# Performance work log

Hardware: AMD Instinct MI355X
Metric: run time of the kernel (lower is better)

## Reference

```python
import jax, jax.numpy as jnp
import numpy as np

B, L, C = 16, 4096, 9          # batch, max chars, max candidate spans per char (2+3+4)
DI, DO, V = 512, 128, 96       # char hidden, attention/pos-embed dim, pos-BEM vocab


def setup_inputs() -> dict:
    key = jax.random.key(0)
    k0, k1, k2, k3, k4, k5 = jax.random.split(key, 6)
    input_context = jax.random.normal(k0, (B, L, DI), jnp.float32)
    W = jax.random.normal(k1, (DO, DI), jnp.float32) / np.sqrt(DI).astype(np.float32)
    pos_embed = jax.random.normal(k2, (V, DO), jnp.float32)
    cand_idx = jax.random.randint(k3, (B, L, C), 0, V, dtype=jnp.int32)
    cand_mask = jax.random.randint(k4, (B, L, C), 0, 2, dtype=jnp.int32).astype(bool)
    word_seq_len = jax.random.randint(k5, (B,), L // 2, L + 1, dtype=jnp.int32)
    return {
        'input_context': input_context,
        'W': W,
        'pos_embed': pos_embed,
        'cand_idx': cand_idx,
        'cand_mask': cand_mask,
        'word_seq_len': word_seq_len,
    }


def reference(input_context, W, pos_embed, cand_idx, cand_mask, word_seq_len):
    # 'general' attention: score_c = cand_c . (W x_char)
    q = jnp.einsum('bld,od->blo', input_context, W)          # [B, L, DO]
    cand = pos_embed[cand_idx]                               # [B, L, C, DO] gather
    scores = jnp.einsum('blco,blo->blc', cand, q)            # [B, L, C]
    neg = jnp.finfo(scores.dtype).min
    attn = jax.nn.softmax(jnp.where(cand_mask, scores, neg), axis=-1)
    ctx = jnp.einsum('blc,blco->blo', attn, cand)            # [B, L, DO]
    # chars with no matched candidate -> zeros(output_size); pad beyond seq_len -> zeros
    has_cand = cand_mask.any(axis=-1, keepdims=True)         # [B, L, 1]
    in_len = jnp.arange(L, dtype=word_seq_len.dtype)[None, :, None] < word_seq_len[:, None, None]
    return jnp.where(has_cand & in_len, ctx, jnp.zeros((), ctx.dtype))
```

## Files before the change

kernel.cpp:

```cpp
#include <hip/hip_runtime.h>
#include <hip/hip_bf16.h>
#include <hip/hip_fp16.h>
#include <cfloat>

#define BB   16
#define LL   4096
#define CC   9
#define DIN  512
#define DOUT 128
#define VV   96

#define PWLD 520
#define PELD 136

typedef _Float16 h2 __attribute__((ext_vector_type(2)));

#if defined(__has_builtin)
#if __has_builtin(__builtin_amdgcn_fdot2)
#define FDOT2(a, b, c) __builtin_amdgcn_fdot2((a), (b), (c), false)
#endif
#endif
#ifndef FDOT2
__device__ __forceinline__ float FDOT2(h2 a, h2 b, float c) {
    return c + (float)a[0] * (float)b[0] + (float)a[1] * (float)b[1];
}
#endif

__device__ __forceinline__ h2 pack_h2(float lo, float hi) {
    return __builtin_bit_cast(h2, __builtin_amdgcn_cvt_pkrtz(lo, hi));
}

__global__ __launch_bounds__(128)
void pw_kernel(const float* __restrict__ W,
               const float* __restrict__ PE,
               __half*      __restrict__ PW)
{
    const int v = blockIdx.x;
    const int k = blockIdx.y * 128 + threadIdx.x;
    const float* per = PE + v * DOUT;
    float a = 0.f;
    #pragma unroll 8
    for (int o = 0; o < DOUT; ++o)
        a = fmaf(per[o], W[(size_t)o * DIN + k], a);
    PW[(size_t)v * DIN + k] = __float2half_rn(a);
}

__global__ __launch_bounds__(256)
void peh_kernel(const float* __restrict__ PE, __half* __restrict__ PEh)
{
    const int i = blockIdx.x * 256 + threadIdx.x;
    float2 f = ((const float2*)PE)[i];
    ((__half2*)PEh)[i] = __floats2half2_rn(f.x, f.y);
}

__global__ __launch_bounds__(1024, 1)
void attn_kernel(const float*  __restrict__ X,
                 const __half* __restrict__ PW,
                 const __half* __restrict__ PEh,
                 const int*    __restrict__ CIDX,
                 const int*    __restrict__ CMASK,
                 const int*    __restrict__ SLEN,
                 float*        __restrict__ OUT)
{
    __shared__ __half lds_pw[VV * PWLD];
    __shared__ __half lds_pe[VV * PELD];

    const int t = threadIdx.x;

    #pragma unroll
    for (int it = 0; it < 6; ++it) {
        int chunk = t + it * 1024;
        int v = chunk >> 6, kq = chunk & 63;
        uint4 d = *(const uint4*)(PW + (size_t)v * DIN + kq * 8);
        *(uint4*)&lds_pw[v * PWLD + kq * 8] = d;
    }
    {
        int v = t >> 4, kq = t & 15;
        if (t < 1536)
            *(uint4*)&lds_pe[v * PELD + kq * 8] =
                *(const uint4*)(PEh + (size_t)v * DOUT + kq * 8);
        int c2 = t + 1024;
        if (c2 < 1536) {
            int v2 = c2 >> 4, k2 = c2 & 15;
            *(uint4*)&lds_pe[v2 * PELD + k2 * 8] =
                *(const uint4*)(PEh + (size_t)v2 * DOUT + k2 * 8);
        }
    }
    __syncthreads();

    const int lane = t & 63;
    const int il   = lane & 15;
    const int slot = t >> 4;
    const int rowbase = blockIdx.x * 128;

    #pragma unroll
    for (int iter = 0; iter < 2; ++iter) {
        const int row = rowbase + iter * 64 + slot;
        const int  b     = row >> 12;
        const int  l     = row & (LL - 1);
        const bool inlen = l < SLEN[b];

        int ci[CC], vmw[CC];
        #pragma unroll
        for (int c = 0; c < CC; ++c) ci[c]  = CIDX[(size_t)row * CC + c];
        #pragma unroll
        for (int c = 0; c < CC; ++c) vmw[c] = CMASK[(size_t)row * CC + c];

        const float* xr = X + (size_t)row * DIN;
        float4 xf[8];
        #pragma unroll
        for (int j = 0; j < 4; ++j) {
            xf[j * 2 + 0] = *(const float4*)(xr + il * 8 + 128 * j);
            xf[j * 2 + 1] = *(const float4*)(xr + il * 8 + 128 * j + 4);
        }
        h2 xh[16];
        #pragma unroll
        for (int q = 0; q < 8; ++q) {
            xh[q * 2 + 0] = pack_h2(xf[q].x, xf[q].y);
            xh[q * 2 + 1] = pack_h2(xf[q].z, xf[q].w);
        }

        float sc[CC];
        #pragma unroll
        for (int c = 0; c < CC; ++c) sc[c] = 0.f;
        #pragma unroll
        for (int j = 0; j < 4; ++j) {
            #pragma unroll
            for (int c = 0; c < CC; ++c) {
                uint4 pwb = *(const uint4*)&lds_pw[ci[c] * PWLD + j * 128 + il * 8];
                h2 p0 = __builtin_bit_cast(h2, pwb.x);
                h2 p1 = __builtin_bit_cast(h2, pwb.y);
                h2 p2 = __builtin_bit_cast(h2, pwb.z);
                h2 p3 = __builtin_bit_cast(h2, pwb.w);
                float s = sc[c];
                s = FDOT2(xh[j * 4 + 0], p0, s);
                s = FDOT2(xh[j * 4 + 1], p1, s);
                s = FDOT2(xh[j * 4 + 2], p2, s);
                s = FDOT2(xh[j * 4 + 3], p3, s);
                sc[c] = s;
            }
        }
        #pragma unroll
        for (int c = 0; c < CC; ++c) {
            float s = sc[c];
            s += __shfl_xor(s, 1);
            s += __shfl_xor(s, 2);
            s += __shfl_xor(s, 4);
            s += __shfl_xor(s, 8);
            sc[c] = s;
        }

        bool any = false;
        float mx = -FLT_MAX;
        #pragma unroll
        for (int c = 0; c < CC; ++c)
            if (vmw[c]) { mx = fmaxf(mx, sc[c]); any = true; }
        float e[CC];
        float den = 0.f;
        #pragma unroll
        for (int c = 0; c < CC; ++c) {
            e[c] = vmw[c] ? __expf(sc[c] - mx) : 0.f;
            den += e[c];
        }
        const float scale = (any && inlen) ? (1.f / den) : 0.f;

        float o[8];
        #pragma unroll
        for (int j = 0; j < 8; ++j) o[j] = 0.f;
        #pragma unroll
        for (int c = 0; c < CC; ++c) {
            const float w = e[c];
            uint4 peb = *(const uint4*)&lds_pe[ci[c] * PELD + il * 8];
            h2 q0 = __builtin_bit_cast(h2, peb.x);
            h2 q1 = __builtin_bit_cast(h2, peb.y);
            h2 q2 = __builtin_bit_cast(h2, peb.z);
            h2 q3 = __builtin_bit_cast(h2, peb.w);
            o[0] = fmaf(w, (float)q0[0], o[0]); o[1] = fmaf(w, (float)q0[1], o[1]);
            o[2] = fmaf(w, (float)q1[0], o[2]); o[3] = fmaf(w, (float)q1[1], o[3]);
            o[4] = fmaf(w, (float)q2[0], o[4]); o[5] = fmaf(w, (float)q2[1], o[5]);
            o[6] = fmaf(w, (float)q3[0], o[6]); o[7] = fmaf(w, (float)q3[1], o[7]);
        }

        float* op = OUT + (size_t)row * DOUT + il * 8;
        *(float4*)op       = make_float4(o[0] * scale, o[1] * scale, o[2] * scale, o[3] * scale);
        *(float4*)(op + 4) = make_float4(o[4] * scale, o[5] * scale, o[6] * scale, o[7] * scale);
    }
}

extern "C" void kernel_launch(void* const* d_in, const int* in_sizes, int n_in,
                              void* d_out, int out_size, void* d_ws, size_t ws_size,
                              hipStream_t stream) {
    const float* X  = (const float*)d_in[0];
    const float* W  = (const float*)d_in[1];
    const float* PE = (const float*)d_in[2];
    const int*   CI = (const int*)d_in[3];
    const int*   CM = (const int*)d_in[4];
    const int*   SL = (const int*)d_in[5];
    float* OUT = (float*)d_out;
    __half* PW  = (__half*)d_ws;
    __half* PEh = (__half*)d_ws + (size_t)VV * DIN;

    hipLaunchKernelGGL(pw_kernel, dim3(VV, 4), dim3(128), 0, stream, W, PE, PW);
    hipLaunchKernelGGL(peh_kernel, dim3((VV * DOUT / 2) / 256), dim3(256), 0, stream, PE, PEh);

    const int rows = BB * LL;
    hipLaunchKernelGGL(attn_kernel, dim3(rows / 128), dim3(1024), 0, stream,
                       X, PW, PEh, CI, CM, SL, OUT);
}
```

Before: 45.24 us.

## Fold PE fp16 conversion into pw_kernel and double-buffer row loads

Merges the PE-to-half conversion into the PW precompute kernel, which removes one kernel launch. The attention kernel now processes 256 rows per block (4 iterations) instead of 128, so each block amortizes its LDS table fill over more rows. It also prefetches the next row's indices, mask and X slice into registers while computing the current row. Launch bounds now request 4 blocks per SM, but each block uses about 126 KB of LDS, so occupancy is probably still limited to one block. The double-buffered registers raise VGPR pressure.

```diff
diff --git a/kernel.cpp b/kernel.cpp
--- a/kernel.cpp
+++ b/kernel.cpp
@@ -33,7 +33,8 @@
 __global__ __launch_bounds__(128)
 void pw_kernel(const float* __restrict__ W,
                const float* __restrict__ PE,
-               __half*      __restrict__ PW)
+               __half*      __restrict__ PW,
+               __half*      __restrict__ PEh)
 {
     const int v = blockIdx.x;
     const int k = blockIdx.y * 128 + threadIdx.x;
@@ -43,17 +44,11 @@
     for (int o = 0; o < DOUT; ++o)
         a = fmaf(per[o], W[(size_t)o * DIN + k], a);
     PW[(size_t)v * DIN + k] = __float2half_rn(a);
-}
-
-__global__ __launch_bounds__(256)
-void peh_kernel(const float* __restrict__ PE, __half* __restrict__ PEh)
-{
-    const int i = blockIdx.x * 256 + threadIdx.x;
-    float2 f = ((const float2*)PE)[i];
-    ((__half2*)PEh)[i] = __floats2half2_rn(f.x, f.y);
-}
-
-__global__ __launch_bounds__(1024, 1)
+    if (blockIdx.y == 0)
+        PEh[(size_t)v * DOUT + threadIdx.x] = __float2half_rn(per[threadIdx.x]);
+}
+
+__global__ __launch_bounds__(1024, 4)
 void attn_kernel(const float*  __restrict__ X,
                  const __half* __restrict__ PW,
                  const __half* __restrict__ PEh,
@@ -75,10 +70,11 @@
         *(uint4*)&lds_pw[v * PWLD + kq * 8] = d;
     }
     {
-        int v = t >> 4, kq = t & 15;
-        if (t < 1536)
+        if (t < 1536) {
+            int v = t >> 4, kq = t & 15;
             *(uint4*)&lds_pe[v * PELD + kq * 8] =
                 *(const uint4*)(PEh + (size_t)v * DOUT + kq * 8);
+        }
         int c2 = t + 1024;
         if (c2 < 1536) {
             int v2 = c2 >> 4, k2 = c2 & 15;
@@ -91,43 +87,65 @@
     const int lane = t & 63;
     const int il   = lane & 15;
     const int slot = t >> 4;
-    const int rowbase = blockIdx.x * 128;
+    const int rowbase = blockIdx.x * 256;
+
+    int    ci[2][CC];
+    int    vmw[2][CC];
+    float4 xf[2][8];
+
+    {
+        const int row = rowbase + slot;
+        #pragma unroll
+        for (int c = 0; c < CC; ++c) ci[0][c]  = CIDX[(size_t)row * CC + c];
+        #pragma unroll
+        for (int c = 0; c < CC; ++c) vmw[0][c] = CMASK[(size_t)row * CC + c];
+        const float* xr = X + (size_t)row * DIN;
+        #pragma unroll
+        for (int j = 0; j < 4; ++j) {
+            xf[0][j * 2 + 0] = *(const float4*)(xr + il * 8 + 128 * j);
+            xf[0][j * 2 + 1] = *(const float4*)(xr + il * 8 + 128 * j + 4);
+        }
+    }
 
     #pragma unroll
-    for (int iter = 0; iter < 2; ++iter) {
-        const int row = rowbase + iter * 64 + slot;
+    for (int i = 0; i < 4; ++i) {
+        const int cur = i & 1;
+        const int nxt = cur ^ 1;
+
+        if (i < 3) {
+            const int rown = rowbase + (i + 1) * 64 + slot;
+            #pragma unroll
+            for (int c = 0; c < CC; ++c) ci[nxt][c]  = CIDX[(size_t)rown * CC + c];
+            #pragma unroll
+            for (int c = 0; c < CC; ++c) vmw[nxt][c] = CMASK[(size_t)rown * CC + c];
+            const float* xrn = X + (size_t)rown * DIN;
+            #pragma unroll
+            for (int j = 0; j < 4; ++j) {
+                xf[nxt][j * 2 + 0] = *(const float4*)(xrn + il * 8 + 128 * j);
+                xf[nxt][j * 2 + 1] = *(const float4*)(xrn + il * 8 + 128 * j + 4);
+            }
+        }
+
+        const int row = rowbase + i * 64 + slot;
         const int  b     = row >> 12;
         const int  l     = row & (LL - 1);
         const bool inlen = l < SLEN[b];
 
-        int ci[CC], vmw[CC];
-        #pragma unroll
-        for (int c = 0; c < CC; ++c) ci[c]  = CIDX[(size_t)row * CC + c];
-        #pragma unroll
-        for (int c = 0; c < CC; ++c) vmw[c] = CMASK[(size_t)row * CC + c];
-
-        const float* xr = X + (size_t)row * DIN;
-        float4 xf[8];
+        h2 xh[16];
+        #pragma unroll
+        for (int q = 0; q < 8; ++q) {
+            xh[q * 2 + 0] = pack_h2(xf[cur][q].x, xf[cur][q].y);
+            xh[q * 2 + 1] = pack_h2(xf[cur][q].z, xf[cur][q].w);
+        }
+
+        float sc[CC];
+        #pragma unroll
+        for (int c = 0; c < CC; ++c) sc[c] = 0.f;
         #pragma unroll
         for (int j = 0; j < 4; ++j) {
-            xf[j * 2 + 0] = *(const float4*)(xr + il * 8 + 128 * j);
-            xf[j * 2 + 1] = *(const float4*)(xr + il * 8 + 128 * j + 4);
-        }
-        h2 xh[16];
-        #pragma unroll
-        for (int q = 0; q < 8; ++q) {
-            xh[q * 2 + 0] = pack_h2(xf[q].x, xf[q].y);
-            xh[q * 2 + 1] = pack_h2(xf[q].z, xf[q].w);
-        }
-
-        float sc[CC];
-        #pragma unroll
-        for (int c = 0; c < CC; ++c) sc[c] = 0.f;
-        #pragma unroll
-        for (int j = 0; j < 4; ++j) {
             #pragma unroll
             for (int c = 0; c < CC; ++c) {
-                uint4 pwb = *(const uint4*)&lds_pw[ci[c] * PWLD + j * 128 + il * 8];
+                uint4 pwb = *(const uint4*)&lds_pw[ci[cur][c] * PWLD + j * 128 + il * 8];
                 h2 p0 = __builtin_bit_cast(h2, pwb.x);
                 h2 p1 = __builtin_bit_cast(h2, pwb.y);
                 h2 p2 = __builtin_bit_cast(h2, pwb.z);
@@ -154,12 +172,12 @@
         float mx = -FLT_MAX;
         #pragma unroll
         for (int c = 0; c < CC; ++c)
-            if (vmw[c]) { mx = fmaxf(mx, sc[c]); any = true; }
+            if (vmw[cur][c]) { mx = fmaxf(mx, sc[c]); any = true; }
         float e[CC];
         float den = 0.f;
         #pragma unroll
         for (int c = 0; c < CC; ++c) {
-            e[c] = vmw[c] ? __expf(sc[c] - mx) : 0.f;
+            e[c] = vmw[cur][c] ? __expf(sc[c] - mx) : 0.f;
             den += e[c];
         }
         const float scale = (any && inlen) ? (1.f / den) : 0.f;
@@ -170,7 +188,7 @@
         #pragma unroll
         for (int c = 0; c < CC; ++c) {
             const float w = e[c];
-            uint4 peb = *(const uint4*)&lds_pe[ci[c] * PELD + il * 8];
+            uint4 peb = *(const uint4*)&lds_pe[ci[cur][c] * PELD + il * 8];
             h2 q0 = __builtin_bit_cast(h2, peb.x);
             h2 q1 = __builtin_bit_cast(h2, peb.y);
             h2 q2 = __builtin_bit_cast(h2, peb.z);
@@ -200,10 +218,9 @@
     __half* PW  = (__half*)d_ws;
     __half* PEh = (__half*)d_ws + (size_t)VV * DIN;
 
-    hipLaunchKernelGGL(pw_kernel, dim3(VV, 4), dim3(128), 0, stream, W, PE, PW);
-    hipLaunchKernelGGL(peh_kernel, dim3((VV * DOUT / 2) / 256), dim3(256), 0, stream, PE, PEh);
+    hipLaunchKernelGGL(pw_kernel, dim3(VV, 4), dim3(128), 0, stream, W, PE, PW, PEh);
 
     const int rows = BB * LL;
-    hipLaunchKernelGGL(attn_kernel, dim3(rows / 128), dim3(1024), 0, stream,
+    hipLaunchKernelGGL(attn_kernel, dim3(rows / 256), dim3(1024), 0, stream,
                        X, PW, PEh, CI, CM, SL, OUT);
 }
```

Measured after the change: 45.81 us. Within noise of the previous version (+1.3%).

## Compute all-vocab scores with MFMA instead of per-candidate fdot2 gathers

Applied to the files above, without the earlier changes.

Replaces the per-candidate gathered fdot2 scoring with a dense MFMA 16x16x32 f16 GEMM of each row against all 96 precomputed PE·W vectors. The scores go to LDS (reusing the PW buffer) and each row's 9 candidates are picked from there. The x loads are software-pipelined with four register buffers, the PE fp16 conversion is folded into pw_kernel, and each block now handles 256 rows. This trades about 10x redundant FLOPs, which the matrix cores absorb, for far fewer scattered LDS reads, at the cost of extra syncs and an LDS round trip for the scores.

```diff
diff --git a/kernel.cpp b/kernel.cpp
--- a/kernel.cpp
+++ b/kernel.cpp
@@ -10,30 +10,23 @@
 #define DOUT 128
 #define VV   96
 
-#define PWLD 520
+#define BLD  536
+#define SLD  97
 #define PELD 136
-
-typedef _Float16 h2 __attribute__((ext_vector_type(2)));
-
-#if defined(__has_builtin)
-#if __has_builtin(__builtin_amdgcn_fdot2)
-#define FDOT2(a, b, c) __builtin_amdgcn_fdot2((a), (b), (c), false)
-#endif
-#endif
-#ifndef FDOT2
-__device__ __forceinline__ float FDOT2(h2 a, h2 b, float c) {
-    return c + (float)a[0] * (float)b[0] + (float)a[1] * (float)b[1];
-}
-#endif
-
-__device__ __forceinline__ h2 pack_h2(float lo, float hi) {
-    return __builtin_bit_cast(h2, __builtin_amdgcn_cvt_pkrtz(lo, hi));
+#define BBYTES (VV * BLD * 2)
+
+typedef _Float16 f16x8 __attribute__((ext_vector_type(8)));
+typedef __attribute__((ext_vector_type(4))) float f32x4;
+
+__device__ __forceinline__ unsigned int pk2(float lo, float hi) {
+    return __builtin_bit_cast(unsigned int, __builtin_amdgcn_cvt_pkrtz(lo, hi));
 }
 
 __global__ __launch_bounds__(128)
 void pw_kernel(const float* __restrict__ W,
                const float* __restrict__ PE,
-               __half*      __restrict__ PW)
+               __half*      __restrict__ PW,
+               __half*      __restrict__ PEh)
 {
     const int v = blockIdx.x;
     const int k = blockIdx.y * 128 + threadIdx.x;
@@ -43,17 +36,11 @@
     for (int o = 0; o < DOUT; ++o)
         a = fmaf(per[o], W[(size_t)o * DIN + k], a);
     PW[(size_t)v * DIN + k] = __float2half_rn(a);
-}
-
-__global__ __launch_bounds__(256)
-void peh_kernel(const float* __restrict__ PE, __half* __restrict__ PEh)
-{
-    const int i = blockIdx.x * 256 + threadIdx.x;
-    float2 f = ((const float2*)PE)[i];
-    ((__half2*)PEh)[i] = __floats2half2_rn(f.x, f.y);
-}
-
-__global__ __launch_bounds__(1024, 1)
+    if (blockIdx.y == 0)
+        PEh[(size_t)v * DOUT + threadIdx.x] = __float2half_rn(per[threadIdx.x]);
+}
+
+__global__ __launch_bounds__(1024)
 void attn_kernel(const float*  __restrict__ X,
                  const __half* __restrict__ PW,
                  const __half* __restrict__ PEh,
@@ -62,128 +49,155 @@
                  const int*    __restrict__ SLEN,
                  float*        __restrict__ OUT)
 {
-    __shared__ __half lds_pw[VV * PWLD];
-    __shared__ __half lds_pe[VV * PELD];
-
-    const int t = threadIdx.x;
+    __shared__ __align__(16) unsigned char lds_raw[BBYTES + VV * PELD * 2];
+    __half* Blds  = (__half*)lds_raw;
+    float*  Slds  = (float*)lds_raw;
+    __half* PElds = (__half*)(lds_raw + BBYTES);
+
+    const int t    = threadIdx.x;
+    const int lane = t & 63;
+    const int fr   = lane & 15;
+    const int q8   = (lane >> 4) * 8;
+    const int wid  = t >> 6;
+    const int row0 = blockIdx.x * 256;
+    const int wrow = row0 + wid * 16 + fr;
+
+    const float* xr = X + (size_t)wrow * DIN + q8;
+
+    float4 A0a, A0b, A1a, A1b, A2a, A2b, A3a, A3b;
+#define ISSUE(BUF, KK) { BUF##a = *(const float4*)(xr + (KK) * 32); \
+                         BUF##b = *(const float4*)(xr + (KK) * 32 + 4); }
+    ISSUE(A0, 0) ISSUE(A1, 1) ISSUE(A2, 2) ISSUE(A3, 3)
 
     #pragma unroll
     for (int it = 0; it < 6; ++it) {
         int chunk = t + it * 1024;
         int v = chunk >> 6, kq = chunk & 63;
         uint4 d = *(const uint4*)(PW + (size_t)v * DIN + kq * 8);
-        *(uint4*)&lds_pw[v * PWLD + kq * 8] = d;
-    }
-    {
+        *(uint4*)&Blds[v * BLD + kq * 8] = d;
+    }
+    if (t < 1536) {
         int v = t >> 4, kq = t & 15;
-        if (t < 1536)
-            *(uint4*)&lds_pe[v * PELD + kq * 8] =
-                *(const uint4*)(PEh + (size_t)v * DOUT + kq * 8);
+        *(uint4*)&PElds[v * PELD + kq * 8] =
+            *(const uint4*)(PEh + (size_t)v * DOUT + kq * 8);
+    }
+    if (t < 512) {
         int c2 = t + 1024;
-        if (c2 < 1536) {
-            int v2 = c2 >> 4, k2 = c2 & 15;
-            *(uint4*)&lds_pe[v2 * PELD + k2 * 8] =
-                *(const uint4*)(PEh + (size_t)v2 * DOUT + k2 * 8);
+        int v2 = c2 >> 4, k2 = c2 & 15;
+        *(uint4*)&PElds[v2 * PELD + k2 * 8] =
+            *(const uint4*)(PEh + (size_t)v2 * DOUT + k2 * 8);
+    }
+    __syncthreads();
+
+    f32x4 acc[6];
+    #pragma unroll
+    for (int nf = 0; nf < 6; ++nf) acc[nf] = (f32x4)0.f;
+
+#define USE(BUF, KK) {                                                        \
+        uint4 up;                                                             \
+        up.x = pk2(BUF##a.x, BUF##a.y); up.y = pk2(BUF##a.z, BUF##a.w);       \
+        up.z = pk2(BUF##b.x, BUF##b.y); up.w = pk2(BUF##b.z, BUF##b.w);       \
+        f16x8 af = __builtin_bit_cast(f16x8, up);                             \
+        _Pragma("unroll")                                                     \
+        for (int nf = 0; nf < 6; ++nf) {                                      \
+            f16x8 bf = *(const f16x8*)&Blds[(nf * 16 + fr) * BLD + (KK) * 32 + q8]; \
+            acc[nf] = __builtin_amdgcn_mfma_f32_16x16x32_f16(af, bf, acc[nf], 0, 0, 0); \
+        }                                                                     \
+    }
+
+    USE(A0, 0)  ISSUE(A0, 4)
+    USE(A1, 1)  ISSUE(A1, 5)
+    USE(A2, 2)  ISSUE(A2, 6)
+    USE(A3, 3)  ISSUE(A3, 7)
+    USE(A0, 4)  ISSUE(A0, 8)
+    USE(A1, 5)  ISSUE(A1, 9)
+    USE(A2, 6)  ISSUE(A2, 10)
+    USE(A3, 7)  ISSUE(A3, 11)
+    USE(A0, 8)  ISSUE(A0, 12)
+    USE(A1, 9)  ISSUE(A1, 13)
+    USE(A2, 10) ISSUE(A2, 14)
+    USE(A3, 11) ISSUE(A3, 15)
+    USE(A0, 12)
+    USE(A1, 13)
+    USE(A2, 14)
+    USE(A3, 15)
+#undef USE
+#undef ISSUE
+
+    const int r_e  = t >> 2;
+    const int sub  = t & 3;
+    const int grow = row0 + r_e;
+    int ci[CC], vmw[CC];
+    #pragma unroll
+    for (int c = 0; c < CC; ++c) ci[c]  = CIDX[(size_t)grow * CC + c];
+    #pragma unroll
+    for (int c = 0; c < CC; ++c) vmw[c] = CMASK[(size_t)grow * CC + c];
+
+    __syncthreads();
+
+    #pragma unroll
+    for (int nf = 0; nf < 6; ++nf) {
+        const int col = nf * 16 + fr;
+        const int rb  = wid * 16 + (lane >> 4) * 4;
+        #pragma unroll
+        for (int j = 0; j < 4; ++j)
+            Slds[(rb + j) * SLD + col] = acc[nf][j];
+    }
+    __syncthreads();
+
+    const int  b     = grow >> 12;
+    const int  l     = grow & (LL - 1);
+    const bool inlen = l < SLEN[b];
+
+    float sc[CC];
+    #pragma unroll
+    for (int c = 0; c < CC; ++c) sc[c] = Slds[r_e * SLD + ci[c]];
+
+    bool any = false;
+    float mx = -FLT_MAX;
+    #pragma unroll
+    for (int c = 0; c < CC; ++c)
+        if (vmw[c]) { mx = fmaxf(mx, sc[c]); any = true; }
+    float e[CC];
+    float den = 0.f;
+    #pragma unroll
+    for (int c = 0; c < CC; ++c) {
+        e[c] = vmw[c] ? __expf(sc[c] - mx) : 0.f;
+        den += e[c];
+    }
+    const float scale = (any && inlen) ? (1.f / den) : 0.f;
+
+    float o[32];
+    #pragma unroll
+    for (int j = 0; j < 32; ++j) o[j] = 0.f;
+    #pragma unroll
+    for (int c = 0; c < CC; ++c) {
+        const float w = e[c];
+        const __half* pe = PElds + ci[c] * PELD + sub * 32;
+        #pragma unroll
+        for (int q = 0; q < 4; ++q) {
+            uint4 u = *(const uint4*)(pe + q * 8);
+            __half2 h0 = __builtin_bit_cast(__half2, u.x);
+            __half2 h1 = __builtin_bit_cast(__half2, u.y);
+            __half2 h2 = __builtin_bit_cast(__half2, u.z);
+            __half2 h3 = __builtin_bit_cast(__half2, u.w);
+            o[q * 8 + 0] = fmaf(w, __half2float(h0.x), o[q * 8 + 0]);
+            o[q * 8 + 1] = fmaf(w, __half2float(h0.y), o[q * 8 + 1]);
+            o[q * 8 + 2] = fmaf(w, __half2float(h1.x), o[q * 8 + 2]);
+            o[q * 8 + 3] = fmaf(w, __half2float(h1.y), o[q * 8 + 3]);
+            o[q * 8 + 4] = fmaf(w, __half2float(h2.x), o[q * 8 + 4]);
+            o[q * 8 + 5] = fmaf(w, __half2float(h2.y), o[q * 8 + 5]);
+            o[q * 8 + 6] = fmaf(w, __half2float(h3.x), o[q * 8 + 6]);
+            o[q * 8 + 7] = fmaf(w, __half2float(h3.y), o[q * 8 + 7]);
         }
     }
-    __syncthreads();
-
-    const int lane = t & 63;
-    const int il   = lane & 15;
-    const int slot = t >> 4;
-    const int rowbase = blockIdx.x * 128;
-
-    #pragma unroll
-    for (int iter = 0; iter < 2; ++iter) {
-        const int row = rowbase + iter * 64 + slot;
-        const int  b     = row >> 12;
-        const int  l     = row & (LL - 1);
-        const bool inlen = l < SLEN[b];
-
-        int ci[CC], vmw[CC];
-        #pragma unroll
-        for (int c = 0; c < CC; ++c) ci[c]  = CIDX[(size_t)row * CC + c];
-        #pragma unroll
-        for (int c = 0; c < CC; ++c) vmw[c] = CMASK[(size_t)row * CC + c];
-
-        const float* xr = X + (size_t)row * DIN;
-        float4 xf[8];
-        #pragma unroll
-        for (int j = 0; j < 4; ++j) {
-            xf[j * 2 + 0] = *(const float4*)(xr + il * 8 + 128 * j);
-            xf[j * 2 + 1] = *(const float4*)(xr + il * 8 + 128 * j + 4);
-        }
-        h2 xh[16];
-        #pragma unroll
-        for (int q = 0; q < 8; ++q) {
-            xh[q * 2 + 0] = pack_h2(xf[q].x, xf[q].y);
-            xh[q * 2 + 1] = pack_h2(xf[q].z, xf[q].w);
-        }
-
-        float sc[CC];
-        #pragma unroll
-        for (int c = 0; c < CC; ++c) sc[c] = 0.f;
-        #pragma unroll
-        for (int j = 0; j < 4; ++j) {
-            #pragma unroll
-            for (int c = 0; c < CC; ++c) {
-                uint4 pwb = *(const uint4*)&lds_pw[ci[c] * PWLD + j * 128 + il * 8];
-                h2 p0 = __builtin_bit_cast(h2, pwb.x);
-                h2 p1 = __builtin_bit_cast(h2, pwb.y);
-                h2 p2 = __builtin_bit_cast(h2, pwb.z);
-                h2 p3 = __builtin_bit_cast(h2, pwb.w);
-                float s = sc[c];
-                s = FDOT2(xh[j * 4 + 0], p0, s);
-                s = FDOT2(xh[j * 4 + 1], p1, s);
-                s = FDOT2(xh[j * 4 + 2], p2, s);
-                s = FDOT2(xh[j * 4 + 3], p3, s);
-                sc[c] = s;
-            }
-        }
-        #pragma unroll
-        for (int c = 0; c < CC; ++c) {
-            float s = sc[c];
-            s += __shfl_xor(s, 1);
-            s += __shfl_xor(s, 2);
-            s += __shfl_xor(s, 4);
-            s += __shfl_xor(s, 8);
-            sc[c] = s;
-        }
-
-        bool any = false;
-        float mx = -FLT_MAX;
-        #pragma unroll
-        for (int c = 0; c < CC; ++c)
-            if (vmw[c]) { mx = fmaxf(mx, sc[c]); any = true; }
-        float e[CC];
-        float den = 0.f;
-        #pragma unroll
-        for (int c = 0; c < CC; ++c) {
-            e[c] = vmw[c] ? __expf(sc[c] - mx) : 0.f;
-            den += e[c];
-        }
-        const float scale = (any && inlen) ? (1.f / den) : 0.f;
-
-        float o[8];
-        #pragma unroll
-        for (int j = 0; j < 8; ++j) o[j] = 0.f;
-        #pragma unroll
-        for (int c = 0; c < CC; ++c) {
-            const float w = e[c];
-            uint4 peb = *(const uint4*)&lds_pe[ci[c] * PELD + il * 8];
-            h2 q0 = __builtin_bit_cast(h2, peb.x);
-            h2 q1 = __builtin_bit_cast(h2, peb.y);
-            h2 q2 = __builtin_bit_cast(h2, peb.z);
-            h2 q3 = __builtin_bit_cast(h2, peb.w);
-            o[0] = fmaf(w, (float)q0[0], o[0]); o[1] = fmaf(w, (float)q0[1], o[1]);
-            o[2] = fmaf(w, (float)q1[0], o[2]); o[3] = fmaf(w, (float)q1[1], o[3]);
-            o[4] = fmaf(w, (float)q2[0], o[4]); o[5] = fmaf(w, (float)q2[1], o[5]);
-            o[6] = fmaf(w, (float)q3[0], o[6]); o[7] = fmaf(w, (float)q3[1], o[7]);
-        }
-
-        float* op = OUT + (size_t)row * DOUT + il * 8;
-        *(float4*)op       = make_float4(o[0] * scale, o[1] * scale, o[2] * scale, o[3] * scale);
-        *(float4*)(op + 4) = make_float4(o[4] * scale, o[5] * scale, o[6] * scale, o[7] * scale);
+
+    float* op = OUT + (size_t)grow * DOUT + sub * 32;
+    #pragma unroll
+    for (int q = 0; q < 8; ++q) {
+        float4 v = make_float4(o[q * 4 + 0] * scale, o[q * 4 + 1] * scale,
+                               o[q * 4 + 2] * scale, o[q * 4 + 3] * scale);
+        *(float4*)(op + q * 4) = v;
     }
 }
 
@@ -200,10 +214,9 @@
     __half* PW  = (__half*)d_ws;
     __half* PEh = (__half*)d_ws + (size_t)VV * DIN;
 
-    hipLaunchKernelGGL(pw_kernel, dim3(VV, 4), dim3(128), 0, stream, W, PE, PW);
-    hipLaunchKernelGGL(peh_kernel, dim3((VV * DOUT / 2) / 256), dim3(256), 0, stream, PE, PEh);
+    hipLaunchKernelGGL(pw_kernel, dim3(VV, 4), dim3(128), 0, stream, W, PE, PW, PEh);
 
     const int rows = BB * LL;
-    hipLaunchKernelGGL(attn_kernel, dim3(rows / 128), dim3(1024), 0, stream,
+    hipLaunchKernelGGL(attn_kernel, dim3(rows / 256), dim3(1024), 0, stream,
                        X, PW, PEh, CI, CM, SL, OUT);
 }
```

Measured after the change: 52.14 us. 1.15x slower.
